# Kernel tuning notes

Measured on AMD Instinct MI355X. Metric: run time of the kernel, lower is better.

## Reference

```python
import jax, jax.numpy as jnp
import numpy as np

B = 8388608  # batch

def moth(x, a, b):
    # per-feature parametric elementwise activation: a * x * sigmoid(b * x)
    return a * x * jax.nn.sigmoid(b * x)

def setup_inputs() -> dict:
    key = jax.random.key(0)
    ks = jax.random.split(key, 12)
    inp = {
        'x':  jax.random.normal(ks[0], (B, 2), dtype=jnp.float32),
        'W1': jax.random.normal(ks[1], (2, 8), dtype=jnp.float32) * (1.0 / np.sqrt(2)),
        'b1': jax.random.normal(ks[2], (8,), dtype=jnp.float32) * 0.01,
        'a1': jax.random.normal(ks[3], (8,), dtype=jnp.float32) * 0.1 + 1.0,
        'c1': jax.random.normal(ks[4], (8,), dtype=jnp.float32) * 0.1 + 1.0,
        'W2': jax.random.normal(ks[5], (8, 4), dtype=jnp.float32) * (1.0 / np.sqrt(8)),
        'b2': jax.random.normal(ks[6], (4,), dtype=jnp.float32) * 0.01,
        'a2': jax.random.normal(ks[7], (4,), dtype=jnp.float32) * 0.1 + 1.0,
        'c2': jax.random.normal(ks[8], (4,), dtype=jnp.float32) * 0.1 + 1.0,
        'W3': jax.random.normal(ks[9], (4, 1), dtype=jnp.float32) * (1.0 / np.sqrt(4)),
        'b3': jax.random.normal(ks[10], (1,), dtype=jnp.float32) * 0.01,
    }
    return inp

def reference(x, W1, b1, a1, c1, W2, b2, a2, c2, W3, b3):
    h = x @ W1 + b1            # [B, 8]
    h = moth(h, a1, c1)        # [B, 8]
    h = h @ W2 + b2            # [B, 4]
    h = moth(h, a2, c2)        # [B, 4]
    out = h @ W3 + b3          # [B, 1]
    return out
```

## Files before the change

kernel.cpp:

```cpp
#include <hip/hip_runtime.h>

#define NLOG2E -1.44269504088896340736f


__global__ void prefold_kernel(
    const float* __restrict__ W1, const float* __restrict__ b1,
    const float* __restrict__ a1, const float* __restrict__ c1,
    const float* __restrict__ W2, const float* __restrict__ b2,
    const float* __restrict__ a2, const float* __restrict__ c2,
    const float* __restrict__ W3, const float* __restrict__ b3,
    float* __restrict__ C)
{
    if (threadIdx.x == 0 && blockIdx.x == 0) {
        for (int j = 0; j < 8; ++j) {
            float ncl = c1[j] * NLOG2E;
            C[j]      = W1[j]     * ncl;
            C[8 + j]  = W1[8 + j] * ncl;
            C[16 + j] = b1[j]     * ncl;
            float k1 = a1[j] / ncl;
            for (int k = 0; k < 4; ++k)
                C[24 + j * 4 + k] = W2[j * 4 + k] * k1;
        }
        for (int k = 0; k < 4; ++k) {
            C[56 + k] = b2[k];
            C[60 + k] = c2[k] * NLOG2E;
            C[64 + k] = a2[k] * W3[k];
        }
        C[68] = b3[0];
    }
}

__global__ __launch_bounds__(256, 4) void PlaygroundModel_66365834658304_kernel(
    const float* __restrict__ x, const float* __restrict__ C,
    float* __restrict__ out, int rows)
{
    int tid = blockIdx.x * blockDim.x + threadIdx.x;
    long long base = (long long)tid * 4;

    const float* uw0  = C;
    const float* uw1  = C + 8;
    const float* ub   = C + 16;
    const float* w2f  = C + 24;
    const float* bb2  = C + 56;
    const float* ncl2 = C + 60;
    const float* aw2  = C + 64;
    float bb3 = C[68];

    if (base + 3 < rows) {
        const float4* x4 = (const float4*)x;
        float4 p0 = x4[(size_t)tid * 2 + 0];
        float4 p1 = x4[(size_t)tid * 2 + 1];
        float X0[4] = {p0.x, p0.z, p1.x, p1.z};
        float X1[4] = {p0.y, p0.w, p1.y, p1.w};

        float u[4][8];
#pragma unroll
        for (int r = 0; r < 4; ++r)
#pragma unroll
            for (int j = 0; j < 8; ++j)
                u[r][j] = fmaf(X0[r], uw0[j], fmaf(X1[r], uw1[j], ub[j]));

#pragma unroll
        for (int r = 0; r < 4; ++r)
#pragma unroll
            for (int j = 0; j < 8; ++j) {
                float e = __builtin_amdgcn_exp2f(u[r][j]);
                float s = __builtin_amdgcn_rcpf(1.0f + e);
                u[r][j] = u[r][j] * s;
            }

        float t2[4][4];
#pragma unroll
        for (int r = 0; r < 4; ++r)
#pragma unroll
            for (int k = 0; k < 4; ++k) {
                float t = bb2[k];
#pragma unroll
                for (int j = 0; j < 8; ++j)
                    t = fmaf(u[r][j], w2f[j * 4 + k], t);
                t2[r][k] = t;
            }

        float s2[4][4];
#pragma unroll
        for (int r = 0; r < 4; ++r)
#pragma unroll
            for (int k = 0; k < 4; ++k) {
                float u2 = ncl2[k] * t2[r][k];
                s2[r][k] = __builtin_amdgcn_rcpf(
                               1.0f + __builtin_amdgcn_exp2f(u2));
            }
        float res[4];
#pragma unroll
        for (int r = 0; r < 4; ++r) {
            float o = bb3;
#pragma unroll
            for (int k = 0; k < 4; ++k)
                o = fmaf(t2[r][k] * s2[r][k], aw2[k], o);
            res[r] = o;
        }
        ((float4*)out)[tid] = make_float4(res[0], res[1], res[2], res[3]);
    } else if (base < rows) {
        for (long long rr = base; rr < rows; ++rr) {
            float x0 = x[rr * 2 + 0], x1 = x[rr * 2 + 1];
            float o = bb3;
            float h[8];
#pragma unroll
            for (int j = 0; j < 8; ++j) {
                float uu = fmaf(x0, uw0[j], fmaf(x1, uw1[j], ub[j]));
                float s  = __builtin_amdgcn_rcpf(
                               1.0f + __builtin_amdgcn_exp2f(uu));
                h[j] = uu * s;
            }
#pragma unroll
            for (int k = 0; k < 4; ++k) {
                float t = bb2[k];
#pragma unroll
                for (int j = 0; j < 8; ++j) t = fmaf(h[j], w2f[j * 4 + k], t);
                float u2 = ncl2[k] * t;
                float sg = __builtin_amdgcn_rcpf(
                               1.0f + __builtin_amdgcn_exp2f(u2));
                o = fmaf(t * sg, aw2[k], o);
            }
            out[rr] = o;
        }
    }
}

extern "C" void kernel_launch(void* const* d_in, const int* in_sizes, int n_in,
                              void* d_out, int out_size, void* d_ws, size_t ws_size,
                              hipStream_t stream) {
    const float* x  = (const float*)d_in[0];
    const float* W1 = (const float*)d_in[1];
    const float* b1 = (const float*)d_in[2];
    const float* a1 = (const float*)d_in[3];
    const float* c1 = (const float*)d_in[4];
    const float* W2 = (const float*)d_in[5];
    const float* b2 = (const float*)d_in[6];
    const float* a2 = (const float*)d_in[7];
    const float* c2 = (const float*)d_in[8];
    const float* W3 = (const float*)d_in[9];
    const float* b3 = (const float*)d_in[10];
    float* out = (float*)d_out;
    float* C   = (float*)d_ws;

    prefold_kernel<<<1, 64, 0, stream>>>(W1, b1, a1, c1, W2, b2, a2, c2,
                                         W3, b3, C);

    int rows  = in_sizes[0] / 2;
    int rows4 = (rows + 3) / 4;
    int block = 256;
    int grid  = (rows4 + block - 1) / block;

    PlaygroundModel_66365834658304_kernel<<<grid, block, 0, stream>>>(
        x, C, out, rows);
}
```

Before: 126.6 us.

## Use persistent grid-stride loop with software-prefetched next input tile

Result: slower. 138.0 us (+9.0%).

```diff
diff --git a/kernel.cpp b/kernel.cpp
--- a/kernel.cpp
+++ b/kernel.cpp
@@ -32,11 +32,8 @@
 
 __global__ __launch_bounds__(256, 4) void PlaygroundModel_66365834658304_kernel(
     const float* __restrict__ x, const float* __restrict__ C,
-    float* __restrict__ out, int rows)
+    float* __restrict__ out, int units, int rows, int T)
 {
-    int tid = blockIdx.x * blockDim.x + threadIdx.x;
-    long long base = (long long)tid * 4;
-
     const float* uw0  = C;
     const float* uw1  = C + 8;
     const float* ub   = C + 16;
@@ -46,27 +43,41 @@
     const float* aw2  = C + 64;
     float bb3 = C[68];
 
-    if (base + 3 < rows) {
-        const float4* x4 = (const float4*)x;
-        float4 p0 = x4[(size_t)tid * 2 + 0];
-        float4 p1 = x4[(size_t)tid * 2 + 1];
-        float X0[4] = {p0.x, p0.z, p1.x, p1.z};
-        float X1[4] = {p0.y, p0.w, p1.y, p1.w};
+    int tid = blockIdx.x * blockDim.x + threadIdx.x;
+    const float4* x4 = (const float4*)x;
+    float4* o4 = (float4*)out;
 
-        float u[4][8];
+    int u = tid;
+    float4 n0, n1;
+    if (u < units) {
+        n0 = x4[(size_t)u * 2 + 0];
+        n1 = x4[(size_t)u * 2 + 1];
+    }
+    while (u < units) {
+        float4 c0 = n0, c1 = n1;
+        int nu = u + T;
+        if (nu < units) {
+            n0 = x4[(size_t)nu * 2 + 0];
+            n1 = x4[(size_t)nu * 2 + 1];
+        }
+
+        float X0[4] = {c0.x, c0.z, c1.x, c1.z};
+        float X1[4] = {c0.y, c0.w, c1.y, c1.w};
+
+        float uv[4][8];
 #pragma unroll
         for (int r = 0; r < 4; ++r)
 #pragma unroll
             for (int j = 0; j < 8; ++j)
-                u[r][j] = fmaf(X0[r], uw0[j], fmaf(X1[r], uw1[j], ub[j]));
+                uv[r][j] = fmaf(X0[r], uw0[j], fmaf(X1[r], uw1[j], ub[j]));
 
 #pragma unroll
         for (int r = 0; r < 4; ++r)
 #pragma unroll
             for (int j = 0; j < 8; ++j) {
-                float e = __builtin_amdgcn_exp2f(u[r][j]);
+                float e = __builtin_amdgcn_exp2f(uv[r][j]);
                 float s = __builtin_amdgcn_rcpf(1.0f + e);
-                u[r][j] = u[r][j] * s;
+                uv[r][j] = uv[r][j] * s;
             }
 
         float t2[4][4];
@@ -77,33 +88,33 @@
                 float t = bb2[k];
 #pragma unroll
                 for (int j = 0; j < 8; ++j)
-                    t = fmaf(u[r][j], w2f[j * 4 + k], t);
+                    t = fmaf(uv[r][j], w2f[j * 4 + k], t);
                 t2[r][k] = t;
             }
 
-        float s2[4][4];
+        float res[4];
 #pragma unroll
-        for (int r = 0; r < 4; ++r)
+        for (int r = 0; r < 4; ++r) {
+            float s2[4];
 #pragma unroll
             for (int k = 0; k < 4; ++k) {
                 float u2 = ncl2[k] * t2[r][k];
-                s2[r][k] = __builtin_amdgcn_rcpf(
-                               1.0f + __builtin_amdgcn_exp2f(u2));
+                s2[k] = __builtin_amdgcn_rcpf(
+                            1.0f + __builtin_amdgcn_exp2f(u2));
             }
-        float res[4];
-#pragma unroll
-        for (int r = 0; r < 4; ++r) {
             float o = bb3;
 #pragma unroll
             for (int k = 0; k < 4; ++k)
-                o = fmaf(t2[r][k] * s2[r][k], aw2[k], o);
+                o = fmaf(t2[r][k] * s2[k], aw2[k], o);
             res[r] = o;
         }
-        ((float4*)out)[tid] = make_float4(res[0], res[1], res[2], res[3]);
-    } else if (base < rows) {
-        for (long long rr = base; rr < rows; ++rr) {
+        o4[u] = make_float4(res[0], res[1], res[2], res[3]);
+        u = nu;
+    }
+
+    if (tid == 0) {
+        for (long long rr = (long long)units * 4; rr < rows; ++rr) {
             float x0 = x[rr * 2 + 0], x1 = x[rr * 2 + 1];
-            float o = bb3;
             float h[8];
 #pragma unroll
             for (int j = 0; j < 8; ++j) {
@@ -112,6 +123,7 @@
                                1.0f + __builtin_amdgcn_exp2f(uu));
                 h[j] = uu * s;
             }
+            float o = bb3;
 #pragma unroll
             for (int k = 0; k < 4; ++k) {
                 float t = bb2[k];
@@ -148,10 +160,11 @@
                                          W3, b3, C);
 
     int rows  = in_sizes[0] / 2;
-    int rows4 = (rows + 3) / 4;
+    int units = rows / 4;
     int block = 256;
-    int grid  = (rows4 + block - 1) / block;
+    int grid  = 1024;
+    int T     = grid * block;
 
     PlaygroundModel_66365834658304_kernel<<<grid, block, 0, stream>>>(
-        x, C, out, rows);
+        x, C, out, units, rows, T);
 }
```
